# Performance work log

Hardware: AMD Instinct MI355X
Metric: run time of the kernel (lower is better)

## Reference

```python
import jax, jax.numpy as jnp
import numpy as np

SCALING = 2.0  # alpha / r = 32 / 16

def setup_inputs() -> dict:
    key = jax.random.key(0)
    k1, k2, k3, k4, k5, k6 = jax.random.split(key, 6)
    B, S, D_IN, D_OUT, R, N_ADAPT = 32, 512, 4096, 4096, 16, 32
    x = jax.random.normal(k1, (B, S, D_IN), dtype=jnp.float32)
    adapter_ids = jax.random.randint(k2, (B,), 0, N_ADAPT)
    A_all = jax.random.normal(k3, (N_ADAPT, R, D_IN), dtype=jnp.float32) * (1.0 / np.sqrt(D_IN))
    B_all = jax.random.normal(k4, (N_ADAPT, D_OUT, R), dtype=jnp.float32) * 0.02
    W = jax.random.normal(k5, (D_OUT, D_IN), dtype=jnp.float32) * (1.0 / np.sqrt(D_IN))
    b = jax.random.normal(k6, (D_OUT,), dtype=jnp.float32) * 0.01
    return {"x": x, "adapter_ids": adapter_ids, "A_all": A_all, "B_all": B_all, "W": W, "b": b}

def reference(x, adapter_ids, A_all, B_all, W, b):
    # base linear: (B,S,D_in) @ (D_in,D_out) + bias
    base_out = jnp.einsum('bsi,oi->bso', x, W) + b
    # per-sample gather of adapter weights (multi-adapter branch)
    A_batch = A_all[adapter_ids]  # (B, rank, D_in)
    B_batch = B_all[adapter_ids]  # (B, D_out, rank)
    intermediate = jnp.einsum('bri,bsi->bsr', A_batch, x)       # (B, S, rank)
    lora_out = jnp.einsum('bor,bsr->bso', B_batch, intermediate)  # (B, S, D_out)
    return base_out + SCALING * lora_out
```

## Files before the change

kernel.cpp:

```cpp
#include <hip/hip_runtime.h>
#include <hip/hip_bf16.h>
#include <stdint.h>


typedef __attribute__((ext_vector_type(8))) short bf16x8;
typedef __attribute__((ext_vector_type(4))) float f32x4;
typedef __attribute__((ext_vector_type(8))) unsigned short ushort8;

#define MM    16384
#define DIN   4096
#define DOUT  4096
#define RR    16
#define NAD   32

__device__ __forceinline__ unsigned short f2bf(float f) {
    union { float f; unsigned int u; } v; v.f = f;
    unsigned int r = (v.u + 0x7FFFu + ((v.u >> 16) & 1u)) >> 16;
    return (unsigned short)r;
}

__device__ __forceinline__ void gld16(const void* g, void* l) {
    __builtin_amdgcn_global_load_lds(
        (const __attribute__((address_space(1))) void*)g,
        (__attribute__((address_space(3))) void*)l,
        16, 0, 0);
}

#define BARRIER() __builtin_amdgcn_s_barrier()
#define LGKM0()   do { asm volatile("s_waitcnt lgkmcnt(0)" ::: "memory"); \
                       __builtin_amdgcn_sched_barrier(0); } while (0)
#define WCNT6()   asm volatile("s_waitcnt vmcnt(6)" ::: "memory")
#define WCNT0()   asm volatile("s_waitcnt vmcnt(0)" ::: "memory")

__global__ __launch_bounds__(256) void cvt_kernel(const float* __restrict__ src,
                                                  unsigned short* __restrict__ dst,
                                                  long n) {
    long i0 = ((long)blockIdx.x * 256 + threadIdx.x) * 8;
    long stride = (long)gridDim.x * 256 * 8;
    for (long i = i0; i < n; i += stride) {
        f32x4 f0 = __builtin_nontemporal_load((const f32x4*)(src + i));
        f32x4 f1 = __builtin_nontemporal_load((const f32x4*)(src + i + 4));
        ushort8 o;
        o[0] = f2bf(f0[0]); o[1] = f2bf(f0[1]); o[2] = f2bf(f0[2]); o[3] = f2bf(f0[3]);
        o[4] = f2bf(f1[0]); o[5] = f2bf(f1[1]); o[6] = f2bf(f1[2]); o[7] = f2bf(f1[3]);
        *(ushort8*)(dst + i) = o;
    }
}

__global__ __launch_bounds__(256) void cvt_ball_kernel(const float* __restrict__ Ball,
                                                       unsigned short* __restrict__ Bbf,
                                                       unsigned short* __restrict__ Zrow) {
    int row = blockIdx.x * 256 + threadIdx.x;
    const float* s = Ball + (size_t)row * RR;
    ushort8 o0, o1, z;
    #pragma unroll
    for (int j = 0; j < 8; ++j) {
        o0[j] = f2bf(__builtin_nontemporal_load(s + j));
        o1[j] = f2bf(__builtin_nontemporal_load(s + 8 + j));
        z[j] = 0;
    }
    ushort8* d = (ushort8*)(Bbf + (size_t)row * 32);
    d[0] = o0; d[1] = o1; d[2] = z; d[3] = z;
    if (row == 0) *(ushort8*)Zrow = z;
}

__global__ __launch_bounds__(256) void inter_kernel(const unsigned short* __restrict__ Xbf,
                                                    const unsigned short* __restrict__ Abf,
                                                    const int* __restrict__ ids,
                                                    unsigned short* __restrict__ Ibf) {
    int tid = threadIdx.x, w = tid >> 6, lane = tid & 63;
    int m0 = blockIdx.x * 64 + w * 16;
    int aid = ids[m0 >> 9];
    int lr = lane & 15, lk = (lane >> 4) * 8;
    const unsigned short* xp = Xbf + (size_t)(m0 + lr) * DIN + lk;
    const unsigned short* ap = Abf + ((size_t)aid * RR + lr) * DIN + lk;
    f32x4 acc = {};
    #pragma unroll 4
    for (int k = 0; k < DIN; k += 32) {
        bf16x8 a  = *(const bf16x8*)(xp + k);
        bf16x8 bb = *(const bf16x8*)(ap + k);
        acc = __builtin_amdgcn_mfma_f32_16x16x32_bf16(a, bb, acc, 0, 0, 0);
    }
    int rbase = m0 + (lane >> 4) * 4;
    #pragma unroll
    for (int r = 0; r < 4; ++r) {
        int m = rbase + r;
        Ibf[(size_t)m * 32 + lr]      = f2bf(acc[r] * 2.0f);
        Ibf[(size_t)m * 32 + 16 + lr] = 0;
    }
}

template<int HT>
__device__ __forceinline__ void stage_half(int t, unsigned short* region, int tid,
    const unsigned short* __restrict__ Xbf, const unsigned short* __restrict__ Wbf,
    const unsigned short* __restrict__ Ibf, const unsigned short* __restrict__ BbfA,
    const unsigned short* __restrict__ Zrow, int m0, int n0) {
    if (t > 64) return;
    #pragma unroll
    for (int j = 0; j < 2; ++j) {
        int r = j * 64 + (tid >> 3);
        int gr;
        if (HT == 0)      gr = r + (r & 64);
        else if (HT == 1) gr = 64 + r + (r & 64);
        else if (HT == 2) gr = ((r >> 5) << 6) | (r & 31);
        else              gr = (((r >> 5) << 6) | (r & 31)) + 32;
        int c = ((tid & 7) ^ (r & 7)) * 8;
        const unsigned short* src;
        if (t < 64) {
            src = (HT <= 1 ? Xbf + (size_t)(m0 + gr) * DIN
                           : Wbf + (size_t)(n0 + gr) * DIN) + (size_t)t * 64 + c;
        } else {
            if (c >= 32) src = Zrow;
            else src = (HT <= 1 ? Ibf + (size_t)(m0 + gr) * 32
                                : BbfA + (size_t)(n0 + gr) * 32) + c;
        }
        gld16(src, region + r * 64 + (tid & 7) * 8);
    }
}

__device__ __forceinline__ void readA(bf16x8 (&A)[4][2], const char* p, int hk16, int xsw) {
    #pragma unroll
    for (int fi = 0; fi < 4; ++fi)
        #pragma unroll
        for (int ks = 0; ks < 2; ++ks)
            A[fi][ks] = *(const bf16x8*)(p + fi * 2048 + ((ks * 64 + hk16) ^ xsw));
}
__device__ __forceinline__ void readB(bf16x8 (&B)[2][2], const char* p, int hk16, int xsw) {
    #pragma unroll
    for (int fj = 0; fj < 2; ++fj)
        #pragma unroll
        for (int ks = 0; ks < 2; ++ks)
            B[fj][ks] = *(const bf16x8*)(p + fj * 2048 + ((ks * 64 + hk16) ^ xsw));
}

template<int RO, int CO>
__device__ __forceinline__ void quad(f32x4 (&acc)[8][4], const bf16x8 (&A)[4][2], const bf16x8 (&B)[2][2]) {
    #pragma unroll
    for (int fi = 0; fi < 4; ++fi)
        #pragma unroll
        for (int fj = 0; fj < 2; ++fj)
            #pragma unroll
            for (int ks = 0; ks < 2; ++ks)
                acc[RO + fi][CO + fj] = __builtin_amdgcn_mfma_f32_16x16x32_bf16(
                    A[fi][ks], B[fj][ks], acc[RO + fi][CO + fj], 0, 0, 0);
}

#define MFMA_PHASE(Q)  do { LGKM0(); __builtin_amdgcn_s_setprio(1); Q; \
                            __builtin_amdgcn_s_setprio(0); } while (0)

__global__ __launch_bounds__(512, 2) void gemm8_kernel(
    const unsigned short* __restrict__ Xbf, const unsigned short* __restrict__ Wbf,
    const unsigned short* __restrict__ Ibf, const unsigned short* __restrict__ Bbf,
    const unsigned short* __restrict__ Zrow,
    const float* __restrict__ bias, const int* __restrict__ ids,
    float* __restrict__ out) {
    __shared__ unsigned short lds[2][2][2][8192];

    int tid = threadIdx.x;
    int bid = blockIdx.x;
    int xcd = bid & 7, q = bid >> 3;
    int bm = q >> 1, bn = 2 * xcd + (q & 1);
    int m0 = bm << 8, n0 = bn << 8;
    int aid = ids[m0 >> 9];
    const unsigned short* BbfA = Bbf + (size_t)aid * DOUT * 32;

    int w = tid >> 6, l = tid & 63;
    int wr = w >> 2, wc = w & 3;
    int lr = l & 15;
    int hk16 = (l >> 4) * 16;
    int xsw = (l & 7) << 4;

    int r0 = tid >> 3;
    int cc = ((tid & 7) ^ (r0 & 7)) * 8;
    int g2 = ((r0 >> 5) << 6) | (r0 & 31);
    const unsigned short* pA0 = Xbf + (size_t)(m0 + r0) * DIN + cc;
    const unsigned short* pA1 = Xbf + (size_t)(m0 + 128 + r0) * DIN + cc;
    const unsigned short* pA2 = Xbf + (size_t)(m0 + 64 + r0) * DIN + cc;
    const unsigned short* pA3 = Xbf + (size_t)(m0 + 192 + r0) * DIN + cc;
    const unsigned short* pB0 = Wbf + (size_t)(n0 + g2) * DIN + cc;
    const unsigned short* pB1 = Wbf + (size_t)(n0 + 128 + g2) * DIN + cc;
    const unsigned short* pB2 = Wbf + (size_t)(n0 + 32 + g2) * DIN + cc;
    const unsigned short* pB3 = Wbf + (size_t)(n0 + 160 + g2) * DIN + cc;
    int dof = tid * 8;

    f32x4 acc[8][4] = {};

    stage_half<0>(0, &lds[0][0][0][0], tid, Xbf, Wbf, Ibf, BbfA, Zrow, m0, n0);
    stage_half<1>(0, &lds[0][0][1][0], tid, Xbf, Wbf, Ibf, BbfA, Zrow, m0, n0);
    stage_half<2>(0, &lds[0][1][0][0], tid, Xbf, Wbf, Ibf, BbfA, Zrow, m0, n0);
    stage_half<3>(0, &lds[0][1][1][0], tid, Xbf, Wbf, Ibf, BbfA, Zrow, m0, n0);
    stage_half<0>(1, &lds[1][0][0][0], tid, Xbf, Wbf, Ibf, BbfA, Zrow, m0, n0);
    stage_half<2>(1, &lds[1][1][0][0], tid, Xbf, Wbf, Ibf, BbfA, Zrow, m0, n0);
    stage_half<3>(1, &lds[1][1][1][0], tid, Xbf, Wbf, Ibf, BbfA, Zrow, m0, n0);
    WCNT6(); BARRIER();

    int rowA = (wr * 64 + lr) * 128;
    int rowB = (wc * 32 + lr) * 128;

    #pragma unroll 2
    for (int t = 0; t < 64; ++t) {
        int b = t & 1;
        const char* A0p = (const char*)&lds[b][0][0][0] + rowA;
        const char* A1p = (const char*)&lds[b][0][1][0] + rowA;
        const char* B0p = (const char*)&lds[b][1][0][0] + rowB;
        const char* B1p = (const char*)&lds[b][1][1][0] + rowB;
        bf16x8 a0[4][2], a1[4][2], fb0[2][2], fb1[2][2];

        readA(a0, A0p, hk16, xsw);
        readB(fb0, B0p, hk16, xsw);
        {
            unsigned short* d = &lds[b ^ 1][0][1][0] + dof;
            if (t < 63) { gld16(pA2 + (size_t)(t + 1) * 64, d);
                          gld16(pA3 + (size_t)(t + 1) * 64, d + 4096); }
            else stage_half<1>(t + 1, &lds[b ^ 1][0][1][0], tid, Xbf, Wbf, Ibf, BbfA, Zrow, m0, n0);
        }
        BARRIER();
        MFMA_PHASE((quad<0, 0>(acc, a0, fb0)));
        BARRIER();

        readB(fb1, B1p, hk16, xsw);
        {
            unsigned short* d = &lds[b][0][0][0] + dof;
            if (t < 62) { gld16(pA0 + (size_t)(t + 2) * 64, d);
                          gld16(pA1 + (size_t)(t + 2) * 64, d + 4096); }
            else stage_half<0>(t + 2, &lds[b][0][0][0], tid, Xbf, Wbf, Ibf, BbfA, Zrow, m0, n0);
        }
        BARRIER();
        MFMA_PHASE((quad<0, 2>(acc, a0, fb1)));
        BARRIER();

        readA(a1, A1p, hk16, xsw);
        {
            unsigned short* d = &lds[b][1][0][0] + dof;
            if (t < 62) { gld16(pB0 + (size_t)(t + 2) * 64, d);
                          gld16(pB1 + (size_t)(t + 2) * 64, d + 4096); }
            else stage_half<2>(t + 2, &lds[b][1][0][0], tid, Xbf, Wbf, Ibf, BbfA, Zrow, m0, n0);
        }
        BARRIER();
        MFMA_PHASE((quad<4, 0>(acc, a1, fb0)));
        BARRIER();

        {
            unsigned short* d = &lds[b][1][1][0] + dof;
            if (t < 62) { gld16(pB2 + (size_t)(t + 2) * 64, d);
                          gld16(pB3 + (size_t)(t + 2) * 64, d + 4096); }
            else stage_half<3>(t + 2, &lds[b][1][1][0], tid, Xbf, Wbf, Ibf, BbfA, Zrow, m0, n0);
        }
        WCNT6();
        BARRIER();
        MFMA_PHASE((quad<4, 2>(acc, a1, fb1)));
        BARRIER();
    }

    WCNT0(); BARRIER();
    {
        const char* A0p = (const char*)&lds[0][0][0][0] + rowA;
        const char* A1p = (const char*)&lds[0][0][1][0] + rowA;
        const char* B0p = (const char*)&lds[0][1][0][0] + rowB;
        const char* B1p = (const char*)&lds[0][1][1][0] + rowB;
        bf16x8 a0[4][2], a1[4][2], fb0[2][2], fb1[2][2];
        readA(a0, A0p, hk16, xsw);
        readB(fb0, B0p, hk16, xsw);
        readB(fb1, B1p, hk16, xsw);
        readA(a1, A1p, hk16, xsw);
        LGKM0();
        quad<0, 0>(acc, a0, fb0);
        quad<0, 2>(acc, a0, fb1);
        quad<4, 0>(acc, a1, fb0);
        quad<4, 2>(acc, a1, fb1);
    }

    #pragma unroll
    for (int cj = 0; cj < 4; ++cj) {
        int col = n0 + wc * 64 + cj * 16 + lr;
        float bv = bias[col];
        #pragma unroll
        for (int ri = 0; ri < 8; ++ri) {
            size_t mrow = (size_t)(m0 + wr * 128 + ri * 16 + (l >> 4) * 4);
            float* op = out + mrow * DOUT + col;
            #pragma unroll
            for (int r = 0; r < 4; ++r)
                __builtin_nontemporal_store(acc[ri][cj][r] + bv, op + (size_t)r * DOUT);
        }
    }
}

extern "C" void kernel_launch(void* const* d_in, const int* in_sizes, int n_in,
                              void* d_out, int out_size, void* d_ws, size_t ws_size,
                              hipStream_t stream) {
    const float* x     = (const float*)d_in[0];
    const int*   ids   = (const int*)d_in[1];
    const float* A_all = (const float*)d_in[2];
    const float* B_all = (const float*)d_in[3];
    const float* W     = (const float*)d_in[4];
    const float* bias  = (const float*)d_in[5];
    float* out = (float*)d_out;

    unsigned short* Xbf  = (unsigned short*)d_ws;
    unsigned short* Wbf  = Xbf + (size_t)MM * DIN;
    unsigned short* Abf  = Wbf + (size_t)DOUT * DIN;
    unsigned short* Bbf  = Abf + (size_t)NAD * RR * DIN;
    unsigned short* Ibf  = Bbf + (size_t)NAD * DOUT * 32;
    unsigned short* Zrow = Ibf + (size_t)MM * 32;

    cvt_kernel<<<8192, 256, 0, stream>>>(x, Xbf, (long)MM * DIN);
    cvt_kernel<<<8192, 256, 0, stream>>>(W, Wbf, (long)DOUT * DIN);
    cvt_kernel<<<1024, 256, 0, stream>>>(A_all, Abf, (long)NAD * RR * DIN);
    cvt_ball_kernel<<<512, 256, 0, stream>>>(B_all, Bbf, Zrow);
    inter_kernel<<<256, 256, 0, stream>>>(Xbf, Abf, ids, Ibf);
    gemm8_kernel<<<1024, 512, 0, stream>>>(Xbf, Wbf, Ibf, Bbf, Zrow, bias, ids, out);
}
```

Baseline: 604.6 us.

## Prefetch next sub-tile LDS fragments during MFMA phases in GEMM main loop

Moves the LDS fragment reads (readA/readB) for the next quadrant so they are issued right after each MFMA batch, before the following barrier, and hoists the first a0/fb0 reads out of the loop, carrying them across iterations. The goal is to overlap LDS read latency with MFMA execution instead of waiting on reads at the start of each phase. Fragment registers now persist across iterations, which raises register pressure under the 2-blocks-per-CU launch bound, and barrier/waitcnt placement is reshuffled (WCNT0 on the last iteration), so getting the synchronisation wrong could create LDS hazards.

After: 599.4 us. About the same (-0.9%).

```diff
diff --git a/kernel.cpp b/kernel.cpp
--- a/kernel.cpp
+++ b/kernel.cpp
@@ -145,9 +145,6 @@
                     A[fi][ks], B[fj][ks], acc[RO + fi][CO + fj], 0, 0, 0);
 }
 
-#define MFMA_PHASE(Q)  do { LGKM0(); __builtin_amdgcn_s_setprio(1); Q; \
-                            __builtin_amdgcn_s_setprio(0); } while (0)
-
 __global__ __launch_bounds__(512, 2) void gemm8_kernel(
     const unsigned short* __restrict__ Xbf, const unsigned short* __restrict__ Wbf,
     const unsigned short* __restrict__ Ibf, const unsigned short* __restrict__ Bbf,
@@ -184,6 +181,7 @@
     int dof = tid * 8;
 
     f32x4 acc[8][4] = {};
+    bf16x8 a0[4][2], a1[4][2], fb0[2][2], fb1[2][2];
 
     stage_half<0>(0, &lds[0][0][0][0], tid, Xbf, Wbf, Ibf, BbfA, Zrow, m0, n0);
     stage_half<1>(0, &lds[0][0][1][0], tid, Xbf, Wbf, Ibf, BbfA, Zrow, m0, n0);
@@ -197,17 +195,13 @@
     int rowA = (wr * 64 + lr) * 128;
     int rowB = (wc * 32 + lr) * 128;
 
+    readA(a0, (const char*)&lds[0][0][0][0] + rowA, hk16, xsw);
+    readB(fb0, (const char*)&lds[0][1][0][0] + rowB, hk16, xsw);
+
     #pragma unroll 2
     for (int t = 0; t < 64; ++t) {
         int b = t & 1;
-        const char* A0p = (const char*)&lds[b][0][0][0] + rowA;
-        const char* A1p = (const char*)&lds[b][0][1][0] + rowA;
-        const char* B0p = (const char*)&lds[b][1][0][0] + rowB;
-        const char* B1p = (const char*)&lds[b][1][1][0] + rowB;
-        bf16x8 a0[4][2], a1[4][2], fb0[2][2], fb1[2][2];
-
-        readA(a0, A0p, hk16, xsw);
-        readB(fb0, B0p, hk16, xsw);
+
         {
             unsigned short* d = &lds[b ^ 1][0][1][0] + dof;
             if (t < 63) { gld16(pA2 + (size_t)(t + 1) * 64, d);
@@ -215,10 +209,13 @@
             else stage_half<1>(t + 1, &lds[b ^ 1][0][1][0], tid, Xbf, Wbf, Ibf, BbfA, Zrow, m0, n0);
         }
         BARRIER();
-        MFMA_PHASE((quad<0, 0>(acc, a0, fb0)));
-        BARRIER();
-
-        readB(fb1, B1p, hk16, xsw);
+        LGKM0();
+        __builtin_amdgcn_s_setprio(1);
+        quad<0, 0>(acc, a0, fb0);
+        __builtin_amdgcn_s_setprio(0);
+        readB(fb1, (const char*)&lds[b][1][1][0] + rowB, hk16, xsw);
+        BARRIER();
+
         {
             unsigned short* d = &lds[b][0][0][0] + dof;
             if (t < 62) { gld16(pA0 + (size_t)(t + 2) * 64, d);
@@ -226,10 +223,13 @@
             else stage_half<0>(t + 2, &lds[b][0][0][0], tid, Xbf, Wbf, Ibf, BbfA, Zrow, m0, n0);
         }
         BARRIER();
-        MFMA_PHASE((quad<0, 2>(acc, a0, fb1)));
-        BARRIER();
-
-        readA(a1, A1p, hk16, xsw);
+        LGKM0();
+        __builtin_amdgcn_s_setprio(1);
+        quad<0, 2>(acc, a0, fb1);
+        __builtin_amdgcn_s_setprio(0);
+        readA(a1, (const char*)&lds[b][0][1][0] + rowA, hk16, xsw);
+        BARRIER();
+
         {
             unsigned short* d = &lds[b][1][0][0] + dof;
             if (t < 62) { gld16(pB0 + (size_t)(t + 2) * 64, d);
@@ -237,7 +237,10 @@
             else stage_half<2>(t + 2, &lds[b][1][0][0], tid, Xbf, Wbf, Ibf, BbfA, Zrow, m0, n0);
         }
         BARRIER();
-        MFMA_PHASE((quad<4, 0>(acc, a1, fb0)));
+        LGKM0();
+        __builtin_amdgcn_s_setprio(1);
+        quad<4, 0>(acc, a1, fb0);
+        __builtin_amdgcn_s_setprio(0);
         BARRIER();
 
         {
@@ -246,29 +249,24 @@
                           gld16(pB3 + (size_t)(t + 2) * 64, d + 4096); }
             else stage_half<3>(t + 2, &lds[b][1][1][0], tid, Xbf, Wbf, Ibf, BbfA, Zrow, m0, n0);
         }
-        WCNT6();
-        BARRIER();
-        MFMA_PHASE((quad<4, 2>(acc, a1, fb1)));
-        BARRIER();
-    }
-
-    WCNT0(); BARRIER();
-    {
-        const char* A0p = (const char*)&lds[0][0][0][0] + rowA;
-        const char* A1p = (const char*)&lds[0][0][1][0] + rowA;
-        const char* B0p = (const char*)&lds[0][1][0][0] + rowB;
-        const char* B1p = (const char*)&lds[0][1][1][0] + rowB;
-        bf16x8 a0[4][2], a1[4][2], fb0[2][2], fb1[2][2];
-        readA(a0, A0p, hk16, xsw);
-        readB(fb0, B0p, hk16, xsw);
-        readB(fb1, B1p, hk16, xsw);
-        readA(a1, A1p, hk16, xsw);
-        LGKM0();
-        quad<0, 0>(acc, a0, fb0);
-        quad<0, 2>(acc, a0, fb1);
-        quad<4, 0>(acc, a1, fb0);
+        if (t == 63) { WCNT0(); } else { WCNT6(); }
+        BARRIER();
+        __builtin_amdgcn_s_setprio(1);
         quad<4, 2>(acc, a1, fb1);
-    }
+        __builtin_amdgcn_s_setprio(0);
+        readA(a0, (const char*)&lds[b ^ 1][0][0][0] + rowA, hk16, xsw);
+        readB(fb0, (const char*)&lds[b ^ 1][1][0][0] + rowB, hk16, xsw);
+        BARRIER();
+    }
+
+    LGKM0();
+    quad<0, 0>(acc, a0, fb0);
+    readB(fb1, (const char*)&lds[0][1][1][0] + rowB, hk16, xsw);
+    readA(a1, (const char*)&lds[0][0][1][0] + rowA, hk16, xsw);
+    LGKM0();
+    quad<0, 2>(acc, a0, fb1);
+    quad<4, 0>(acc, a1, fb0);
+    quad<4, 2>(acc, a1, fb1);
 
     #pragma unroll
     for (int cj = 0; cj < 4; ++cj) {
```
